# Kernel optimization log

Measured on AMD Instinct MI355X. Metric: run time of the kernel, lower is better.

## Reference

```python
import jax, jax.numpy as jnp
import numpy as np

VOCAB, IMG_EMB, EMB, HID, P = 10000, 1024, 512, 512, 49
B, T = 64, 50


def setup_inputs() -> dict:
    key = jax.random.key(0)
    ks = jax.random.split(key, 16)
    def lin(k, fin, fout):
        k1, k2 = jax.random.split(k)
        s = 1.0 / np.sqrt(fin)
        return (jax.random.uniform(k1, (fin, fout), minval=-s, maxval=s),
                jax.random.uniform(k2, (fout,), minval=-s, maxval=s))
    Wv, bv = lin(ks[0], IMG_EMB, EMB)
    Wh, bh = lin(ks[1], EMB, HID)
    Wm, bm = lin(ks[2], EMB, HID)
    Wl, bl = lin(ks[3], 2 * EMB + HID, 5 * HID)  # LSTM fc on cat([w_t, vg, h])
    Wav, bav = lin(ks[4], HID, HID)
    Wah, bah = lin(ks[5], HID, HID)
    Was, bas = lin(ks[6], HID, HID)
    Waz, baz = lin(ks[7], HID, 1)
    Wp, bp = lin(ks[8], HID, VOCAB)
    emb = jax.random.normal(ks[9], (VOCAB, EMB)) * 0.02
    return {
        'v': jax.random.normal(ks[10], (B, P, IMG_EMB)),
        'w': jax.random.randint(ks[11], (B, T), 0, VOCAB),
        'lengths': jax.random.randint(ks[12], (B,), 0, T),
        'emb': emb,
        'Wv': Wv, 'bv': bv, 'Wh': Wh, 'bh': bh, 'Wm': Wm, 'bm': bm,
        'Wl': Wl, 'bl': bl,
        'Wav': Wav, 'bav': bav, 'Wah': Wah, 'bah': bah,
        'Was': Was, 'bas': bas, 'Waz': Waz, 'baz': baz,
        'Wp': Wp, 'bp': bp,
    }


def reference(v, w, lengths, emb, Wv, bv, Wh, bh, Wm, bm, Wl, bl,
              Wav, bav, Wah, bah, Was, bas, Waz, baz, Wp, bp):
    we = emb[w]                        # [B,T,E] word embeddings
    v = v @ Wv + bv                    # [B,P,E] projected visual features
    vg = v.mean(axis=1)                # [B,E] global visual feature
    h0 = vg @ Wh + bh                  # [B,H]
    m0 = vg @ Wm + bm                  # [B,H]
    pv = v @ Wav + bav                 # precompute attention proj of v [B,P,H]

    def step(carry, wt):
        h_, m_ = carry
        x = jnp.concatenate([wt, vg, h_], axis=-1)        # [B, 2E+H]
        i, f, o, g, m5 = jnp.split(x @ Wl + bl, 5, axis=-1)
        i = jax.nn.sigmoid(i)
        f = jax.nn.sigmoid(f)
        o = jax.nn.sigmoid(o)
        m = i * jnp.tanh(m5) + f * m_
        tm = jnp.tanh(m)
        h = o * tm
        s = g * tm                                        # sentinel gate
        # adaptive attention over P regions + sentinel h slot
        ph = (h @ Wah + bah)[:, None, :]                  # [B,1,H]
        ps = (s @ Was + bas)[:, None, :]                  # [B,1,H]
        z = jnp.tanh(jnp.concatenate([pv, ph], axis=1) + ps)  # [B,P+1,H]
        a = jax.nn.softmax(z @ Waz + baz, axis=1)         # [B,P+1,1]
        c = jnp.sum(a * jnp.concatenate([v, h[:, None, :]], axis=1), axis=1)
        p = jax.nn.softmax((c + h) @ Wp + bp, axis=-1)    # [B,V]
        return (h, m), p

    _, ps = jax.lax.scan(step, (h0, m0), jnp.swapaxes(we, 0, 1))
    ps = jnp.swapaxes(ps, 0, 1)                           # [B,T,V]
    mask = jnp.arange(ps.shape[1])[None, :] < lengths[:, None]
    return ps * mask[..., None].astype(ps.dtype)
```

## Files before the change

kernel.cpp:

```cpp
#include <hip/hip_runtime.h>
#include <hip/hip_bf16.h>
#include <cstdint>
#include <cstddef>

#define Bn 64
#define Tn 50
#define Pn 49
#define En 512
#define Hn 512
#define Vn 10000
#define IEn 1024
#define G5 2560

typedef __attribute__((ext_vector_type(8))) short bf16x8;
typedef __attribute__((ext_vector_type(4))) float f32x4;

__device__ __forceinline__ float sigm(float x)  { return 1.0f / (1.0f + __expf(-x)); }
__device__ __forceinline__ float tanh_f(float x){ return 1.0f - 2.0f / (1.0f + __expf(2.0f * x)); }

__device__ __forceinline__ unsigned short f2b(float f) {
    union { float f; unsigned int u; } c; c.f = f;
    unsigned int u = c.u;
    u += 0x7fffu + ((u >> 16) & 1u);
    return (unsigned short)(u >> 16);
}
__device__ __forceinline__ float b2f(unsigned short u) {
    union { unsigned int u; float f; } c; c.u = ((unsigned int)u) << 16;
    return c.f;
}

template<bool GATHER>
__global__ __launch_bounds__(256)
void gemm64(const float* __restrict__ A, int lda,
            const float* __restrict__ B,
            float* __restrict__ C,
            int M, int N, int K,
            const float* __restrict__ bias,
            const float* __restrict__ rowadd, int rowDiv, long rowStride,
            const int* __restrict__ gidx)
{
    const int n0 = blockIdx.x * 64;
    const int m0 = blockIdx.y * 64;
    const long koff = (long)blockIdx.z * K;
    const float* Bp = B + koff * N;
    float* Cp = C + (gridDim.z > 1 ? (size_t)blockIdx.z * (size_t)M * (size_t)N : (size_t)0);

    __shared__ float As[16][64];
    __shared__ float Bs[16][64];

    const int tid = threadIdx.x;
    const int tx = tid & 15;
    const int ty = tid >> 4;
    const int ra = tid >> 2;
    const int ca = (tid & 3) << 2;

    long arow = GATHER ? (long)gidx[m0 + ra] : (long)(m0 + ra);
    const float* Arow = A + arow * (long)lda + koff + ca;

    const int kl = ty;
    const int nb = tx << 2;
    const int ncol = n0 + nb;

    float acc[4][4] = {{0.f,0.f,0.f,0.f},{0.f,0.f,0.f,0.f},{0.f,0.f,0.f,0.f},{0.f,0.f,0.f,0.f}};

    for (int k0 = 0; k0 < K; k0 += 16) {
        float4 av = *(const float4*)(Arow + k0);
        float4 bv;
        const float* bptr = Bp + (long)(k0 + kl) * N + ncol;
        if (ncol + 3 < N) {
            bv = *(const float4*)bptr;
        } else {
            bv.x = (ncol + 0 < N) ? bptr[0] : 0.f;
            bv.y = (ncol + 1 < N) ? bptr[1] : 0.f;
            bv.z = (ncol + 2 < N) ? bptr[2] : 0.f;
            bv.w = (ncol + 3 < N) ? bptr[3] : 0.f;
        }
        __syncthreads();
        As[ca + 0][ra] = av.x; As[ca + 1][ra] = av.y;
        As[ca + 2][ra] = av.z; As[ca + 3][ra] = av.w;
        *(float4*)&Bs[kl][nb] = bv;
        __syncthreads();
        #pragma unroll
        for (int kk = 0; kk < 16; kk++) {
            const float4 a = *(const float4*)&As[kk][ty << 2];
            const float4 b = *(const float4*)&Bs[kk][tx << 2];
            const float a_[4] = {a.x, a.y, a.z, a.w};
            const float b_[4] = {b.x, b.y, b.z, b.w};
            #pragma unroll
            for (int i = 0; i < 4; i++)
                #pragma unroll
                for (int j = 0; j < 4; j++)
                    acc[i][j] = fmaf(a_[i], b_[j], acc[i][j]);
        }
    }

    #pragma unroll
    for (int i = 0; i < 4; i++) {
        const int rr = m0 + (ty << 2) + i;
        #pragma unroll
        for (int j = 0; j < 4; j++) {
            const int cc = n0 + (tx << 2) + j;
            if (cc < N) {
                float v = acc[i][j];
                if (bias)   v += bias[cc];
                if (rowadd) v += rowadd[(long)(rr / rowDiv) * rowStride + cc];
                Cp[(long)rr * N + cc] = v;
            }
        }
    }
}

template<int OUTF, int OUTB, int GM, int SWZ>
__global__ __launch_bounds__(256)
void gemm_mfma(const unsigned short* __restrict__ A,
               const unsigned short* __restrict__ BT,
               float* __restrict__ Cf, unsigned short* __restrict__ Cb,
               int M, int N, int K,
               const float* __restrict__ bias,
               const float* __restrict__ rowadd, int rowDiv,
               const int* __restrict__ ridx, const int* __restrict__ dcnt,
               int mtiles)
{
    __shared__ __align__(16) unsigned short Asm[128][40];
    __shared__ __align__(16) unsigned short Bsm[128][40];

    int Meff = M;
    if (GM) Meff = *dcnt;
    int m0, n0;
    if (SWZ) {
        const int nwg = gridDim.x;
        const int q = nwg >> 3, rm = nwg & 7;
        const int xcd = blockIdx.x & 7, pos = blockIdx.x >> 3;
        const int swz = (xcd < rm ? xcd * (q + 1) : rm * (q + 1) + (xcd - rm) * q) + pos;
        m0 = (swz % mtiles) * 128;
        n0 = (swz / mtiles) * 128;
    } else {
        n0 = blockIdx.x * 128;
        m0 = blockIdx.y * 128;
    }
    if (GM && m0 >= Meff) return;

    const int tid = threadIdx.x;
    const int lane = tid & 63;
    const int wid = tid >> 6;
    const int wm = wid >> 1;
    const int wn = wid & 1;

    const int r0 = tid >> 2;
    const int kg = tid & 3;

    const int ar0 = m0 + r0, ar1 = m0 + r0 + 64;
    const int br0 = n0 + r0, br1 = n0 + r0 + 64;
    long arow0, arow1;
    if (GM) {
        arow0 = (ar0 < Meff) ? (long)ridx[ar0] : 0;
        arow1 = (ar1 < Meff) ? (long)ridx[ar1] : 0;
    } else {
        arow0 = ar0; arow1 = ar1;
    }

    f32x4 acc[4][4] = {};
    const uint4 zero4 = {0u, 0u, 0u, 0u};

    uint4 a0, a1, b0, b1;
    {
        const long ka = (long)kg * 8;
        a0 = (GM || ar0 < Meff) ? *(const uint4*)(A + arow0 * K + ka) : zero4;
        a1 = (GM || ar1 < Meff) ? *(const uint4*)(A + arow1 * K + ka) : zero4;
        b0 = (br0 < N) ? *(const uint4*)(BT + (long)br0 * K + ka) : zero4;
        b1 = (br1 < N) ? *(const uint4*)(BT + (long)br1 * K + ka) : zero4;
    }

    for (int k0 = 0; k0 < K; k0 += 32) {
        __syncthreads();
        *(uint4*)&Asm[r0     ][kg * 8] = a0;
        *(uint4*)&Asm[r0 + 64][kg * 8] = a1;
        *(uint4*)&Bsm[r0     ][kg * 8] = b0;
        *(uint4*)&Bsm[r0 + 64][kg * 8] = b1;
        __syncthreads();

        if (k0 + 32 < K) {
            const long ka = (long)(k0 + 32) + kg * 8;
            a0 = (GM || ar0 < Meff) ? *(const uint4*)(A + arow0 * K + ka) : zero4;
            a1 = (GM || ar1 < Meff) ? *(const uint4*)(A + arow1 * K + ka) : zero4;
            b0 = (br0 < N) ? *(const uint4*)(BT + (long)br0 * K + ka) : zero4;
            b1 = (br1 < N) ? *(const uint4*)(BT + (long)br1 * K + ka) : zero4;
        }

        bf16x8 af[4], bfr[4];
        const int arow = wm * 64 + (lane & 15);
        const int brow = wn * 64 + (lane & 15);
        const int kcol = (lane >> 4) * 8;
        #pragma unroll
        for (int i = 0; i < 4; i++) {
            af[i]  = *(const bf16x8*)&Asm[arow + i * 16][kcol];
            bfr[i] = *(const bf16x8*)&Bsm[brow + i * 16][kcol];
        }
        #pragma unroll
        for (int mi = 0; mi < 4; mi++)
            #pragma unroll
            for (int ni = 0; ni < 4; ni++)
                acc[mi][ni] = __builtin_amdgcn_mfma_f32_16x16x32_bf16(af[mi], bfr[ni], acc[mi][ni], 0, 0, 0);
    }

    const int crow = m0 + wm * 64 + (lane >> 4) * 4;
    const int ccol0 = n0 + wn * 64 + (lane & 15);
    #pragma unroll
    for (int ni = 0; ni < 4; ni++) {
        const int col = ccol0 + ni * 16;
        if (col >= N) continue;
        const float bvv = bias ? bias[col] : 0.f;
        #pragma unroll
        for (int mi = 0; mi < 4; mi++) {
            #pragma unroll
            for (int r = 0; r < 4; r++) {
                const int rr = crow + mi * 16 + r;
                if (rr < Meff) {
                    const long orow = GM ? (long)ridx[rr] : (long)rr;
                    float v = acc[mi][ni][r] + bvv;
                    if (rowadd) v += rowadd[(long)(rr / rowDiv) * N + col];
                    if (OUTF) Cf[orow * N + col] = v;
                    if (OUTB) Cb[orow * N + col] = f2b(v);
                }
            }
        }
    }
}

__global__ __launch_bounds__(256)
void transpose_bf16(const float* __restrict__ in, unsigned short* __restrict__ out,
                    int K, int N, int istride)
{
    __shared__ float tile[32][33];
    const int k0 = blockIdx.y * 32;
    const int n0 = blockIdx.x * 32;
    const int tx = threadIdx.x & 31, ty = threadIdx.x >> 5;
    #pragma unroll
    for (int j = 0; j < 4; j++) {
        int k = k0 + ty + j * 8, n = n0 + tx;
        tile[ty + j * 8][tx] = (k < K && n < N) ? in[(long)k * istride + n] : 0.f;
    }
    __syncthreads();
    #pragma unroll
    for (int j = 0; j < 4; j++) {
        int n = n0 + ty + j * 8, k = k0 + tx;
        if (n < N && k < K) out[(long)n * K + k] = f2b(tile[tx][ty + j * 8]);
    }
}

__global__ __launch_bounds__(256)
void transpose3_bf16(const float* __restrict__ A0, const float* __restrict__ A1,
                     const float* __restrict__ A2,
                     unsigned short* __restrict__ O0, unsigned short* __restrict__ O1,
                     unsigned short* __restrict__ O2)
{
    const float* in = (blockIdx.z == 0) ? A0 : (blockIdx.z == 1) ? A1 : A2;
    unsigned short* out = (blockIdx.z == 0) ? O0 : (blockIdx.z == 1) ? O1 : O2;
    __shared__ float tile[32][33];
    const int k0 = blockIdx.y * 32;
    const int n0 = blockIdx.x * 32;
    const int tx = threadIdx.x & 31, ty = threadIdx.x >> 5;
    #pragma unroll
    for (int j = 0; j < 4; j++)
        tile[ty + j * 8][tx] = in[(long)(k0 + ty + j * 8) * 512 + n0 + tx];
    __syncthreads();
    #pragma unroll
    for (int j = 0; j < 4; j++)
        out[(long)(n0 + ty + j * 8) * 512 + k0 + tx] = f2b(tile[tx][ty + j * 8]);
}

__global__ void convert_bf16(const float* __restrict__ in, unsigned short* __restrict__ out, int n4)
{
    int i = blockIdx.x * 256 + threadIdx.x;
    if (i < n4) {
        float4 v = ((const float4*)in)[i];
        ushort4 u;
        u.x = f2b(v.x); u.y = f2b(v.y); u.z = f2b(v.z); u.w = f2b(v.w);
        ((ushort4*)out)[i] = u;
    }
}

__global__ void gather_convert(const float* __restrict__ emb, const int* __restrict__ w,
                               unsigned short* __restrict__ out)
{
    const int r = blockIdx.x;
    const long row = w[r];
    const float4 v = ((const float4*)(emb + row * 512))[threadIdx.x];
    ushort4 u;
    u.x = f2b(v.x); u.y = f2b(v.y); u.z = f2b(v.z); u.w = f2b(v.w);
    ((ushort4*)(out + (long)r * 512))[threadIdx.x] = u;
}

__global__ void compact_rows(const int* __restrict__ len, int* __restrict__ ridx, int* __restrict__ dcnt)
{
    const int b = threadIdx.x;
    int L = len[b]; L = L < 0 ? 0 : (L > Tn ? Tn : L);
    int off = L;
    #pragma unroll
    for (int s = 1; s < 64; s <<= 1) {
        int n = __shfl_up(off, s);
        if (b >= s) off += n;
    }
    const int start = off - L;
    if (b == 63) *dcnt = off;
    for (int t = 0; t < L; t++) ridx[start + t] = b * Tn + t;
}

__global__ void vg_mean(const unsigned short* __restrict__ vproj, float* __restrict__ vg)
{
    const int tid = blockIdx.x * 256 + threadIdx.x;
    const int b = tid >> 9, e = tid & 511;
    const unsigned short* p = vproj + (long)b * Pn * En + e;
    float s = 0.f;
    #pragma unroll 7
    for (int q = 0; q < Pn; q++) s += b2f(p[q * En]);
    vg[tid] = s * (1.0f / 49.0f);
}

__global__ void h0m0(const float* __restrict__ vg,
                     const float* __restrict__ Wh, const float* __restrict__ bh,
                     const float* __restrict__ Wm, const float* __restrict__ bm,
                     unsigned short* __restrict__ h0b, float* __restrict__ m)
{
    __shared__ float vgs[512];
    const int b = blockIdx.x, e = threadIdx.x;
    vgs[e] = vg[b * 512 + e];
    __syncthreads();
    float a1 = bh[e], a2 = bm[e];
    #pragma unroll 8
    for (int k = 0; k < 512; k++) {
        const float x = vgs[k];
        a1 = fmaf(x, Wh[(long)k * 512 + e], a1);
        a2 = fmaf(x, Wm[(long)k * 512 + e], a2);
    }
    h0b[b * 512 + e] = f2b(a1);
    m[b * 512 + e] = a2;
}

__global__ __launch_bounds__(256)
void scan_step(int t, const float* __restrict__ base,
               const unsigned short* __restrict__ hcur,
               unsigned short* __restrict__ hnxt,
               float* __restrict__ mF,
               const unsigned short* __restrict__ W3T,
               float* __restrict__ HsF, unsigned short* __restrict__ Hsb,
               unsigned short* __restrict__ Ssb)
{
    __shared__ __align__(16) unsigned short Wh_s[5][8][520];

    const int tid = threadIdx.x;
    const int lane = tid & 63, wv = tid >> 6;
    const int e0 = blockIdx.x * 8;
    const int col = lane & 15;
    const int fk = (lane >> 4) * 8;
    const int bb = wv * 16 + (lane & 15);

    bf16x8 Ah[16];
    #pragma unroll
    for (int ch = 0; ch < 16; ch++)
        Ah[ch] = *(const bf16x8*)(hcur + (long)bb * 512 + ch * 32 + fk);

    for (int idx = tid; idx < 40 * 64; idx += 256) {
        const int row = idx >> 6, seg = idx & 63;
        const int g = row >> 3, c = row & 7;
        *(uint4*)&Wh_s[g][c][seg * 8] =
            *(const uint4*)(W3T + (long)(g * 512 + e0 + c) * 512 + seg * 8);
    }

    const int rbase = wv * 16 + (lane >> 4) * 4;
    const int ecol = e0 + (col & 7);
    float bse[5][4], mv[4];
    if (col < 8) {
        #pragma unroll
        for (int r = 0; r < 4; r++) {
            const long rrow = (long)(rbase + r) * Tn + t;
            const float* bp = base + rrow * G5 + ecol;
            bse[0][r] = bp[0];    bse[1][r] = bp[512];  bse[2][r] = bp[1024];
            bse[3][r] = bp[1536]; bse[4][r] = bp[2048];
            mv[r] = mF[(rbase + r) * 512 + ecol];
        }
    }

    __syncthreads();

    const unsigned short* B0 = &Wh_s[(col >> 3)    ][col & 7][0];
    const unsigned short* B1 = &Wh_s[2 + (col >> 3)][col & 7][0];
    const unsigned short* B2 = &Wh_s[4][col & 7][0];

    f32x4 a0 = {}, a1 = {}, a2 = {};
    #pragma unroll
    for (int ch = 0; ch < 16; ch++) {
        const int ko = ch * 32 + fk;
        a0 = __builtin_amdgcn_mfma_f32_16x16x32_bf16(Ah[ch], *(const bf16x8*)(B0 + ko), a0, 0, 0, 0);
        a1 = __builtin_amdgcn_mfma_f32_16x16x32_bf16(Ah[ch], *(const bf16x8*)(B1 + ko), a1, 0, 0, 0);
        a2 = __builtin_amdgcn_mfma_f32_16x16x32_bf16(Ah[ch], *(const bf16x8*)(B2 + ko), a2, 0, 0, 0);
    }

    #pragma unroll
    for (int r = 0; r < 4; r++) {
        const float fsh = __shfl_xor(a0[r], 8);
        const float gsh = __shfl_xor(a1[r], 8);
        if (col < 8) {
            const int b = rbase + r;
            const float gi = a0[r] + bse[0][r];
            const float gf = fsh   + bse[1][r];
            const float go = a1[r] + bse[2][r];
            const float gg = gsh   + bse[3][r];
            const float g5 = a2[r] + bse[4][r];
            const float iv = sigm(gi), fv = sigm(gf), ov = sigm(go);
            const float mn = fmaf(iv, tanh_f(g5), fv * mv[r]);
            const float tm = tanh_f(mn);
            const float hh = ov * tm, ss = gg * tm;
            const unsigned short hhi = f2b(hh);
            const long hoff = (long)b * 512 + ecol;
            const long rrow = (long)b * Tn + t;
            mF[hoff] = mn;
            hnxt[hoff] = hhi;
            HsF[rrow * 512 + ecol] = hh;
            Hsb[rrow * 512 + ecol] = hhi;
            Ssb[rrow * 512 + ecol] = f2b(ss);
        }
    }
}

__global__ __launch_bounds__(256)
void attn(const unsigned short* __restrict__ vproj, const float* __restrict__ pv,
          const float* __restrict__ PH, const float* __restrict__ PS,
          const float* __restrict__ Hs, const float* __restrict__ Waz,
          const float* __restrict__ baz, unsigned short* __restrict__ CHb,
          const int* __restrict__ len)
{
    const int r = blockIdx.x;
    const int b = r / Tn;
    if ((r % Tn) >= len[b]) return;
    const int tid = threadIdx.x;
    const int lane = tid & 63, wid = tid >> 6;

    __shared__ float ps_s[512];
    __shared__ float ph_s[512];
    __shared__ float alog[64];

    for (int i = tid; i < 512; i += 256) {
        ps_s[i] = PS[(long)r * 512 + i];
        ph_s[i] = PH[(long)r * 512 + i];
    }
    __syncthreads();

    const float4 wz0 = *(const float4*)(Waz + lane * 8);
    const float4 wz1 = *(const float4*)(Waz + lane * 8 + 4);
    const float4 q0  = *(const float4*)&ps_s[lane * 8];
    const float4 q1  = *(const float4*)&ps_s[lane * 8 + 4];

    for (int slot = wid; slot < Pn + 1; slot += 4) {
        const float* src = (slot < Pn) ? (pv + ((long)b * Pn + slot) * 512)
                                       : (const float*)ph_s;
        const float4 x0 = *(const float4*)(src + lane * 8);
        const float4 x1 = *(const float4*)(src + lane * 8 + 4);
        float d = 0.f;
        d = fmaf(tanh_f(x0.x + q0.x), wz0.x, d);
        d = fmaf(tanh_f(x0.y + q0.y), wz0.y, d);
        d = fmaf(tanh_f(x0.z + q0.z), wz0.z, d);
        d = fmaf(tanh_f(x0.w + q0.w), wz0.w, d);
        d = fmaf(tanh_f(x1.x + q1.x), wz1.x, d);
        d = fmaf(tanh_f(x1.y + q1.y), wz1.y, d);
        d = fmaf(tanh_f(x1.z + q1.z), wz1.z, d);
        d = fmaf(tanh_f(x1.w + q1.w), wz1.w, d);
        #pragma unroll
        for (int s = 32; s >= 1; s >>= 1) d += __shfl_xor(d, s);
        if (lane == 0) alog[slot] = d + baz[0];
    }
    __syncthreads();

    if (wid == 0) {
        const float v = (lane < Pn + 1) ? alog[lane] : -3.4e38f;
        float mx = v;
        #pragma unroll
        for (int s = 32; s >= 1; s >>= 1) mx = fmaxf(mx, __shfl_xor(mx, s));
        const float ev = (lane < Pn + 1) ? __expf(v - mx) : 0.f;
        float sm = ev;
        #pragma unroll
        for (int s = 32; s >= 1; s >>= 1) sm += __shfl_xor(sm, s);
        if (lane < Pn + 1) alog[lane] = ev / sm;
    }
    __syncthreads();

    const float a49 = alog[Pn];
    for (int ee = tid; ee < 512; ee += 256) {
        const float hval = Hs[(long)r * 512 + ee];
        float c = a49 * hval;
        const unsigned short* vp = vproj + (long)b * Pn * 512 + ee;
        #pragma unroll 7
        for (int q = 0; q < Pn; q++) c = fmaf(alog[q], b2f(vp[q * 512]), c);
        CHb[(long)r * 512 + ee] = f2b(c + hval);
    }
}

__global__ __launch_bounds__(256)
void softmax_mask(float* __restrict__ out, const int* __restrict__ lengths)
{
    const int r = blockIdx.x, b = r / Tn, t = r % Tn;
    float* row = out + (long)r * Vn;
    const int tid = threadIdx.x;
    float4* row4 = (float4*)row;

    if (t >= lengths[b]) {
        f32x4* rowv = (f32x4*)row;
        const f32x4 z = {0.f, 0.f, 0.f, 0.f};
        for (int i = tid; i < Vn / 4; i += 256)
            __builtin_nontemporal_store(z, &rowv[i]);
        return;
    }

    __shared__ float red[4];
    const int lane = tid & 63, wid = tid >> 6;

    float4 rv[10];
    float mx = -3.4e38f;
    #pragma unroll
    for (int j = 0; j < 10; j++) {
        const int i = tid + j * 256;
        if (i < Vn / 4) {
            rv[j] = row4[i];
            mx = fmaxf(mx, fmaxf(fmaxf(rv[j].x, rv[j].y), fmaxf(rv[j].z, rv[j].w)));
        }
    }
    #pragma unroll
    for (int s = 32; s >= 1; s >>= 1) mx = fmaxf(mx, __shfl_xor(mx, s));
    if (lane == 0) red[wid] = mx;
    __syncthreads();
    mx = fmaxf(fmaxf(red[0], red[1]), fmaxf(red[2], red[3]));
    __syncthreads();

    float sm = 0.f;
    #pragma unroll
    for (int j = 0; j < 10; j++) {
        const int i = tid + j * 256;
        if (i < Vn / 4) {
            rv[j].x = __expf(rv[j].x - mx);
            rv[j].y = __expf(rv[j].y - mx);
            rv[j].z = __expf(rv[j].z - mx);
            rv[j].w = __expf(rv[j].w - mx);
            sm += rv[j].x + rv[j].y + rv[j].z + rv[j].w;
        }
    }
    #pragma unroll
    for (int s = 32; s >= 1; s >>= 1) sm += __shfl_xor(sm, s);
    if (lane == 0) red[wid] = sm;
    __syncthreads();
    sm = red[0] + red[1] + red[2] + red[3];
    const float inv = 1.0f / sm;

    #pragma unroll
    for (int j = 0; j < 10; j++) {
        const int i = tid + j * 256;
        if (i < Vn / 4) {
            rv[j].x *= inv; rv[j].y *= inv; rv[j].z *= inv; rv[j].w *= inv;
            row4[i] = rv[j];
        }
    }
}

extern "C" void kernel_launch(void* const* d_in, const int* in_sizes, int n_in,
                              void* d_out, int out_size, void* d_ws, size_t ws_size,
                              hipStream_t stream)
{
    (void)in_sizes; (void)n_in; (void)out_size; (void)ws_size;
    const float* v   = (const float*)d_in[0];
    const int*   w   = (const int*)  d_in[1];
    const int*   len = (const int*)  d_in[2];
    const float* emb = (const float*)d_in[3];
    const float* Wv  = (const float*)d_in[4];
    const float* bv  = (const float*)d_in[5];
    const float* Wh  = (const float*)d_in[6];
    const float* bh  = (const float*)d_in[7];
    const float* Wm  = (const float*)d_in[8];
    const float* bm  = (const float*)d_in[9];
    const float* Wl  = (const float*)d_in[10];
    const float* bl  = (const float*)d_in[11];
    const float* Wav = (const float*)d_in[12];
    const float* bav = (const float*)d_in[13];
    const float* Wah = (const float*)d_in[14];
    const float* bah = (const float*)d_in[15];
    const float* Was = (const float*)d_in[16];
    const float* bas = (const float*)d_in[17];
    const float* Waz = (const float*)d_in[18];
    const float* baz = (const float*)d_in[19];
    const float* Wp  = (const float*)d_in[20];
    const float* bp  = (const float*)d_in[21];
    float* out_f = (float*)d_out;

    char* wsp = (char*)d_ws;
    size_t off = 0;
    auto walloc = [&](size_t bytes) -> void* {
        void* r = wsp + off;
        off += (bytes + 255) & ~(size_t)255;
        return r;
    };
    unsigned short* WpT    = (unsigned short*)walloc((size_t)Vn * 512 * 2);
    unsigned short* WvT    = (unsigned short*)walloc((size_t)512 * 1024 * 2);
    unsigned short* WlT0   = (unsigned short*)walloc((size_t)G5 * 512 * 2);
    unsigned short* WavT   = (unsigned short*)walloc((size_t)512 * 512 * 2);
    unsigned short* WahT   = (unsigned short*)walloc((size_t)512 * 512 * 2);
    unsigned short* WasT   = (unsigned short*)walloc((size_t)512 * 512 * 2);
    unsigned short* vprojb = (unsigned short*)walloc((size_t)3136 * 512 * 2);
    unsigned short* CHb    = (unsigned short*)walloc((size_t)3200 * 512 * 2);
    float* vg   = (float*)walloc((size_t)64 * 512 * 4);
    unsigned short* hB = (unsigned short*)walloc((size_t)2 * 64 * 512 * 2);
    float* mbuf = (float*)walloc((size_t)64 * 512 * 4);
    float* vgw  = (float*)walloc((size_t)64 * G5 * 4);
    int*   ridx = (int*)walloc((size_t)3200 * 4);
    int*   dcnt = (int*)walloc(256);

    char* sp = (char*)(out_f + (size_t)3200 * G5);
    size_t off2 = 0;
    auto salloc = [&](size_t bytes) -> void* {
        void* r = sp + off2;
        off2 += (bytes + 255) & ~(size_t)255;
        return r;
    };
    unsigned short* vB  = (unsigned short*)salloc((size_t)3136 * 1024 * 2);
    unsigned short* WEb = (unsigned short*)salloc((size_t)3200 * 512 * 2);
    float* pvb = (float*)salloc((size_t)3136 * 512 * 4);
    float* HsF = (float*)salloc((size_t)3200 * 512 * 4);
    unsigned short* Hsb = (unsigned short*)salloc((size_t)3200 * 512 * 2);
    unsigned short* Ssb = (unsigned short*)salloc((size_t)3200 * 512 * 2);
    float* PHb = (float*)salloc((size_t)3200 * 512 * 4);
    float* PSb = (float*)salloc((size_t)3200 * 512 * 4);
    unsigned short* W3T = (unsigned short*)salloc((size_t)G5 * 512 * 2);

    transpose_bf16<<<dim3(512/32, 1024/32), 256, 0, stream>>>(Wv, WvT, 1024, 512, 512);
    transpose_bf16<<<dim3(G5/32, 512/32), 256, 0, stream>>>(Wl, WlT0, 512, G5, G5);
    transpose3_bf16<<<dim3(16, 16, 3), 256, 0, stream>>>(Wav, Wah, Was, WavT, WahT, WasT);
    transpose_bf16<<<dim3((Vn + 31)/32, 16), 256, 0, stream>>>(Wp, WpT, 512, Vn, Vn);
    transpose_bf16<<<dim3(G5/32, 16), 256, 0, stream>>>(Wl + (size_t)1024 * G5, W3T, 512, G5, G5);
    convert_bf16<<<(3136*1024/4 + 255)/256, 256, 0, stream>>>(v, vB, 3136*1024/4);
    gather_convert<<<3200, 128, 0, stream>>>(emb, w, WEb);
    compact_rows<<<1, 64, 0, stream>>>(len, ridx, dcnt);

    gemm_mfma<0,1,0,0><<<dim3(4, 25), 256, 0, stream>>>(vB, WvT, nullptr, vprojb,
                                                        3136, 512, 1024, bv, nullptr, 1,
                                                        nullptr, nullptr, 0);
    vg_mean<<<128, 256, 0, stream>>>(vprojb, vg);
    h0m0<<<64, 512, 0, stream>>>(vg, Wh, bh, Wm, bm, hB, mbuf);
    gemm64<false><<<dim3(40, 1, 1), 256, 0, stream>>>(vg, 512, Wl + (size_t)512 * G5, vgw,
                                                      64, G5, 512, bl, nullptr, 1, 0, nullptr);
    gemm_mfma<1,0,0,0><<<dim3(4, 25), 256, 0, stream>>>(vprojb, WavT, pvb, nullptr,
                                                        3136, 512, 512, bav, nullptr, 1,
                                                        nullptr, nullptr, 0);
    gemm_mfma<1,0,0,1><<<500, 256, 0, stream>>>(WEb, WlT0, out_f, nullptr,
                                                3200, G5, 512, nullptr, vgw, Tn,
                                                nullptr, nullptr, 25);
    for (int t = 0; t < Tn; t++) {
        const size_t cur = (size_t)(t & 1) * (64 * 512);
        const size_t nxt = (size_t)((t + 1) & 1) * (64 * 512);
        scan_step<<<64, 256, 0, stream>>>(t, out_f, hB + cur, hB + nxt, mbuf, W3T,
                                          HsF, Hsb, Ssb);
    }
    gemm_mfma<1,0,1,0><<<dim3(4, 25), 256, 0, stream>>>(Hsb, WahT, PHb, nullptr,
                                                        3200, 512, 512, bah, nullptr, 1,
                                                        ridx, dcnt, 0);
    gemm_mfma<1,0,1,0><<<dim3(4, 25), 256, 0, stream>>>(Ssb, WasT, PSb, nullptr,
                                                        3200, 512, 512, bas, nullptr, 1,
                                                        ridx, dcnt, 0);
    attn<<<3200, 256, 0, stream>>>(vprojb, pvb, PHb, PSb, HsF, Waz, baz, CHb, len);
    gemm_mfma<1,0,1,1><<<1975, 256, 0, stream>>>(CHb, WpT, out_f, nullptr,
                                                 3200, Vn, 512, bp, nullptr, 1,
                                                 ridx, dcnt, 25);
    softmax_mask<<<3200, 256, 0, stream>>>(out_f, len);
}
```

Measured before the change: 799.7 us.

## Fuse fp32-to-bf16 conversion and embedding gather into MFMA GEMM A-loads

The GEMM kernel can now read fp32 A directly, converting to bf16 in registers, and can optionally gather A rows through an index array. This removes the separate convert_bf16 pass over v and the gather_convert pass over the embeddings, along with their intermediate buffers. The K tile is also widened from 32 to 64 with more padded LDS and four rows per thread, halving the number of barrier iterations. The cost is heavier fp32 global loads and conversion inside the GEMM, plus more registers and LDS per block.

```diff
diff --git a/kernel.cpp b/kernel.cpp
--- a/kernel.cpp
+++ b/kernel.cpp
@@ -27,6 +27,14 @@
 __device__ __forceinline__ float b2f(unsigned short u) {
     union { unsigned int u; float f; } c; c.u = ((unsigned int)u) << 16;
     return c.f;
+}
+__device__ __forceinline__ uint4 pack8(float4 a, float4 b) {
+    uint4 r;
+    r.x = (unsigned)f2b(a.x) | ((unsigned)f2b(a.y) << 16);
+    r.y = (unsigned)f2b(a.z) | ((unsigned)f2b(a.w) << 16);
+    r.z = (unsigned)f2b(b.x) | ((unsigned)f2b(b.y) << 16);
+    r.w = (unsigned)f2b(b.z) | ((unsigned)f2b(b.w) << 16);
+    return r;
 }
 
 template<bool GATHER>
@@ -110,19 +118,22 @@
     }
 }
 
-template<int OUTF, int OUTB, int GM, int SWZ>
+template<int OUTF, int OUTB, int GM, int SWZ, int AF32>
 __global__ __launch_bounds__(256)
-void gemm_mfma(const unsigned short* __restrict__ A,
+void gemm_mfma(const void* __restrict__ Av,
                const unsigned short* __restrict__ BT,
                float* __restrict__ Cf, unsigned short* __restrict__ Cb,
                int M, int N, int K,
                const float* __restrict__ bias,
                const float* __restrict__ rowadd, int rowDiv,
                const int* __restrict__ ridx, const int* __restrict__ dcnt,
-               int mtiles)
-{
-    __shared__ __align__(16) unsigned short Asm[128][40];
-    __shared__ __align__(16) unsigned short Bsm[128][40];
+               int mtiles, const int* __restrict__ agidx)
+{
+    __shared__ __align__(16) unsigned short Asm[128][72];
+    __shared__ __align__(16) unsigned short Bsm[128][72];
+
+    const float* Af = (const float*)Av;
+    const unsigned short* Ab = (const unsigned short*)Av;
 
     int Meff = M;
     if (GM) Meff = *dcnt;
@@ -146,61 +157,80 @@
     const int wm = wid >> 1;
     const int wn = wid & 1;
 
-    const int r0 = tid >> 2;
-    const int kg = tid & 3;
-
-    const int ar0 = m0 + r0, ar1 = m0 + r0 + 64;
-    const int br0 = n0 + r0, br1 = n0 + r0 + 64;
-    long arow0, arow1;
-    if (GM) {
-        arow0 = (ar0 < Meff) ? (long)ridx[ar0] : 0;
-        arow1 = (ar1 < Meff) ? (long)ridx[ar1] : 0;
-    } else {
-        arow0 = ar0; arow1 = ar1;
+    const int r0 = tid >> 3;
+    const int kg8 = (tid & 7) * 8;
+
+    long arow[4];
+    bool avalid[4], bvalid[4];
+    #pragma unroll
+    for (int j = 0; j < 4; j++) {
+        const int ar = m0 + r0 + j * 32;
+        const int br = n0 + r0 + j * 32;
+        if (GM) {
+            avalid[j] = true;
+            arow[j] = (ar < Meff) ? (long)ridx[ar] : 0;
+        } else if (agidx) {
+            avalid[j] = (ar < M);
+            arow[j] = avalid[j] ? (long)agidx[ar] : 0;
+        } else {
+            avalid[j] = (ar < M);
+            arow[j] = avalid[j] ? ar : 0;
+        }
+        bvalid[j] = (br < N);
     }
 
     f32x4 acc[4][4] = {};
     const uint4 zero4 = {0u, 0u, 0u, 0u};
 
-    uint4 a0, a1, b0, b1;
-    {
-        const long ka = (long)kg * 8;
-        a0 = (GM || ar0 < Meff) ? *(const uint4*)(A + arow0 * K + ka) : zero4;
-        a1 = (GM || ar1 < Meff) ? *(const uint4*)(A + arow1 * K + ka) : zero4;
-        b0 = (br0 < N) ? *(const uint4*)(BT + (long)br0 * K + ka) : zero4;
-        b1 = (br1 < N) ? *(const uint4*)(BT + (long)br1 * K + ka) : zero4;
-    }
-
-    for (int k0 = 0; k0 < K; k0 += 32) {
+    uint4 aR[4], bR[4];
+    auto loadAB = [&](int k0) {
+        #pragma unroll
+        for (int j = 0; j < 4; j++) {
+            if (avalid[j]) {
+                if (AF32) {
+                    const float* p = Af + arow[j] * K + k0 + kg8;
+                    aR[j] = pack8(*(const float4*)p, *(const float4*)(p + 4));
+                } else {
+                    aR[j] = *(const uint4*)(Ab + arow[j] * K + k0 + kg8);
+                }
+            } else aR[j] = zero4;
+            bR[j] = bvalid[j] ? *(const uint4*)(BT + (long)(n0 + r0 + j * 32) * K + k0 + kg8)
+                              : zero4;
+        }
+    };
+
+    loadAB(0);
+
+    const int arowf = wm * 64 + (lane & 15);
+    const int browf = wn * 64 + (lane & 15);
+    const int kcol = (lane >> 4) * 8;
+
+    for (int k0 = 0; k0 < K; k0 += 64) {
         __syncthreads();
-        *(uint4*)&Asm[r0     ][kg * 8] = a0;
-        *(uint4*)&Asm[r0 + 64][kg * 8] = a1;
-        *(uint4*)&Bsm[r0     ][kg * 8] = b0;
-        *(uint4*)&Bsm[r0 + 64][kg * 8] = b1;
+        #pragma unroll
+        for (int j = 0; j < 4; j++) {
+            *(uint4*)&Asm[r0 + j * 32][kg8] = aR[j];
+            *(uint4*)&Bsm[r0 + j * 32][kg8] = bR[j];
+        }
         __syncthreads();
 
-        if (k0 + 32 < K) {
-            const long ka = (long)(k0 + 32) + kg * 8;
-            a0 = (GM || ar0 < Meff) ? *(const uint4*)(A + arow0 * K + ka) : zero4;
-            a1 = (GM || ar1 < Meff) ? *(const uint4*)(A + arow1 * K + ka) : zero4;
-            b0 = (br0 < N) ? *(const uint4*)(BT + (long)br0 * K + ka) : zero4;
-            b1 = (br1 < N) ? *(const uint4*)(BT + (long)br1 * K + ka) : zero4;
-        }
-
-        bf16x8 af[4], bfr[4];
-        const int arow = wm * 64 + (lane & 15);
-        const int brow = wn * 64 + (lane & 15);
-        const int kcol = (lane >> 4) * 8;
-        #pragma unroll
-        for (int i = 0; i < 4; i++) {
-            af[i]  = *(const bf16x8*)&Asm[arow + i * 16][kcol];
-            bfr[i] = *(const bf16x8*)&Bsm[brow + i * 16][kcol];
-        }
-        #pragma unroll
-        for (int mi = 0; mi < 4; mi++)
+        if (k0 + 64 < K) loadAB(k0 + 64);
+
+        #pragma unroll
+        for (int h = 0; h < 2; h++) {
+            bf16x8 af[4], bfr[4];
+            const int kc = h * 32 + kcol;
             #pragma unroll
-            for (int ni = 0; ni < 4; ni++)
-                acc[mi][ni] = __builtin_amdgcn_mfma_f32_16x16x32_bf16(af[mi], bfr[ni], acc[mi][ni], 0, 0, 0);
+            for (int i = 0; i < 4; i++) {
+                af[i]  = *(const bf16x8*)&Asm[arowf + i * 16][kc];
+                bfr[i] = *(const bf16x8*)&Bsm[browf + i * 16][kc];
+            }
+            #pragma unroll
+            for (int mi = 0; mi < 4; mi++)
+                #pragma unroll
+                for (int ni = 0; ni < 4; ni++)
+                    acc[mi][ni] = __builtin_amdgcn_mfma_f32_16x16x32_bf16(af[mi], bfr[ni], acc[mi][ni], 0, 0, 0);
+        }
     }
 
     const int crow = m0 + wm * 64 + (lane >> 4) * 4;
@@ -267,28 +297,6 @@
     #pragma unroll
     for (int j = 0; j < 4; j++)
         out[(long)(n0 + ty + j * 8) * 512 + k0 + tx] = f2b(tile[tx][ty + j * 8]);
-}
-
-__global__ void convert_bf16(const float* __restrict__ in, unsigned short* __restrict__ out, int n4)
-{
-    int i = blockIdx.x * 256 + threadIdx.x;
-    if (i < n4) {
-        float4 v = ((const float4*)in)[i];
-        ushort4 u;
-        u.x = f2b(v.x); u.y = f2b(v.y); u.z = f2b(v.z); u.w = f2b(v.w);
-        ((ushort4*)out)[i] = u;
-    }
-}
-
-__global__ void gather_convert(const float* __restrict__ emb, const int* __restrict__ w,
-                               unsigned short* __restrict__ out)
-{
-    const int r = blockIdx.x;
-    const long row = w[r];
-    const float4 v = ((const float4*)(emb + row * 512))[threadIdx.x];
-    ushort4 u;
-    u.x = f2b(v.x); u.y = f2b(v.y); u.z = f2b(v.z); u.w = f2b(v.w);
-    ((ushort4*)(out + (long)r * 512))[threadIdx.x] = u;
 }
 
 __global__ void compact_rows(const int* __restrict__ len, int* __restrict__ ridx, int* __restrict__ dcnt)
@@ -618,8 +626,6 @@
         off2 += (bytes + 255) & ~(size_t)255;
         return r;
     };
-    unsigned short* vB  = (unsigned short*)salloc((size_t)3136 * 1024 * 2);
-    unsigned short* WEb = (unsigned short*)salloc((size_t)3200 * 512 * 2);
     float* pvb = (float*)salloc((size_t)3136 * 512 * 4);
     float* HsF = (float*)salloc((size_t)3200 * 512 * 4);
     unsigned short* Hsb = (unsigned short*)salloc((size_t)3200 * 512 * 2);
@@ -633,38 +639,36 @@
     transpose3_bf16<<<dim3(16, 16, 3), 256, 0, stream>>>(Wav, Wah, Was, WavT, WahT, WasT);
     transpose_bf16<<<dim3((Vn + 31)/32, 16), 256, 0, stream>>>(Wp, WpT, 512, Vn, Vn);
     transpose_bf16<<<dim3(G5/32, 16), 256, 0, stream>>>(Wl + (size_t)1024 * G5, W3T, 512, G5, G5);
-    convert_bf16<<<(3136*1024/4 + 255)/256, 256, 0, stream>>>(v, vB, 3136*1024/4);
-    gather_convert<<<3200, 128, 0, stream>>>(emb, w, WEb);
     compact_rows<<<1, 64, 0, stream>>>(len, ridx, dcnt);
 
-    gemm_mfma<0,1,0,0><<<dim3(4, 25), 256, 0, stream>>>(vB, WvT, nullptr, vprojb,
-                                                        3136, 512, 1024, bv, nullptr, 1,
-                                                        nullptr, nullptr, 0);
+    gemm_mfma<0,1,0,0,1><<<dim3(4, 25), 256, 0, stream>>>(v, WvT, nullptr, vprojb,
+                                                          3136, 512, 1024, bv, nullptr, 1,
+                                                          nullptr, nullptr, 0, nullptr);
     vg_mean<<<128, 256, 0, stream>>>(vprojb, vg);
     h0m0<<<64, 512, 0, stream>>>(vg, Wh, bh, Wm, bm, hB, mbuf);
     gemm64<false><<<dim3(40, 1, 1), 256, 0, stream>>>(vg, 512, Wl + (size_t)512 * G5, vgw,
                                                       64, G5, 512, bl, nullptr, 1, 0, nullptr);
-    gemm_mfma<1,0,0,0><<<dim3(4, 25), 256, 0, stream>>>(vprojb, WavT, pvb, nullptr,
-                                                        3136, 512, 512, bav, nullptr, 1,
-                                                        nullptr, nullptr, 0);
-    gemm_mfma<1,0,0,1><<<500, 256, 0, stream>>>(WEb, WlT0, out_f, nullptr,
-                                                3200, G5, 512, nullptr, vgw, Tn,
-                                                nullptr, nullptr, 25);
+    gemm_mfma<1,0,0,0,0><<<dim3(4, 25), 256, 0, stream>>>(vprojb, WavT, pvb, nullptr,
+                                                          3136, 512, 512, bav, nullptr, 1,
+                                                          nullptr, nullptr, 0, nullptr);
+    gemm_mfma<1,0,0,1,1><<<500, 256, 0, stream>>>(emb, WlT0, out_f, nullptr,
+                                                  3200, G5, 512, nullptr, vgw, Tn,
+                                                  nullptr, nullptr, 25, w);
     for (int t = 0; t < Tn; t++) {
         const size_t cur = (size_t)(t & 1) * (64 * 512);
         const size_t nxt = (size_t)((t + 1) & 1) * (64 * 512);
         scan_step<<<64, 256, 0, stream>>>(t, out_f, hB + cur, hB + nxt, mbuf, W3T,
                                           HsF, Hsb, Ssb);
     }
-    gemm_mfma<1,0,1,0><<<dim3(4, 25), 256, 0, stream>>>(Hsb, WahT, PHb, nullptr,
-                                                        3200, 512, 512, bah, nullptr, 1,
-                                                        ridx, dcnt, 0);
-    gemm_mfma<1,0,1,0><<<dim3(4, 25), 256, 0, stream>>>(Ssb, WasT, PSb, nullptr,
-                                                        3200, 512, 512, bas, nullptr, 1,
-                                                        ridx, dcnt, 0);
+    gemm_mfma<1,0,1,0,0><<<dim3(4, 25), 256, 0, stream>>>(Hsb, WahT, PHb, nullptr,
+                                                          3200, 512, 512, bah, nullptr, 1,
+                                                          ridx, dcnt, 0, nullptr);
+    gemm_mfma<1,0,1,0,0><<<dim3(4, 25), 256, 0, stream>>>(Ssb, WasT, PSb, nullptr,
+                                                          3200, 512, 512, bas, nullptr, 1,
+                                                          ridx, dcnt, 0, nullptr);
     attn<<<3200, 256, 0, stream>>>(vprojb, pvb, PHb, PSb, HsF, Waz, baz, CHb, len);
-    gemm_mfma<1,0,1,1><<<1975, 256, 0, stream>>>(CHb, WpT, out_f, nullptr,
-                                                 3200, Vn, 512, bp, nullptr, 1,
-                                                 ridx, dcnt, 25);
+    gemm_mfma<1,0,1,1,0><<<1975, 256, 0, stream>>>(CHb, WpT, out_f, nullptr,
+                                                   3200, Vn, 512, bp, nullptr, 1,
+                                                   ridx, dcnt, 25, nullptr);
     softmax_mask<<<3200, 256, 0, stream>>>(out_f, len);
 }
```

Result: slower. 968.0 us (+21.0%).
